# Optimization experiments

Hardware: AMD Instinct MI355X
Metric: run time of the kernel (lower is better)

## Reference

```python
import jax, jax.numpy as jnp
import numpy as np

N_NODES = 50000
N_EDGES = 1_280_000
NODE_D = 13
EDGE_RAW_D = 1
H = 64
CONCAT_D = 2 * NODE_D + EDGE_RAW_D  # 27
NEG_SLOPE = 0.2


def _leaky(x):
    return jnp.where(x >= 0, x, NEG_SLOPE * x)


def _scatter_mean(vals, idx, num_nodes):
    # vals: [E, H]; idx: [E] int -> [num_nodes, H] mean over incident edges (0 if none)
    s = jax.ops.segment_sum(vals, idx, num_segments=num_nodes)
    cnt = jax.ops.segment_sum(jnp.ones((vals.shape[0], 1), vals.dtype), idx, num_segments=num_nodes)
    return s / jnp.maximum(cnt, 1.0)


def _conv(e, src, dst, num_nodes, w_self, b_self, w_in, w_out):
    h_self = e @ w_self + b_self
    agg_in = _scatter_mean(e, dst, num_nodes)[src]   # incoming-edge mean at src nodes
    agg_out = _scatter_mean(e, src, num_nodes)[dst]  # outgoing-edge mean at dst nodes
    return _leaky(h_self + agg_in @ w_in + agg_out @ w_out)


def setup_inputs() -> dict:
    key = jax.random.key(0)
    ks = jax.random.split(key, 24)

    def lin(k, fan_in, fan_out):
        return jax.random.normal(k, (fan_in, fan_out), jnp.float32) / np.sqrt(fan_in)

    inp = {
        'x': jax.random.normal(ks[0], (N_NODES, NODE_D), jnp.float32),
        'edge_index': jax.random.randint(ks[1], (2, N_EDGES), 0, N_NODES, jnp.int32),
        'raw_edge_attr': jax.random.normal(ks[2], (N_EDGES, EDGE_RAW_D), jnp.float32),
        'enc_w': lin(ks[3], CONCAT_D, H),
        'enc_b': jnp.zeros((H,), jnp.float32),
    }
    for i, base in zip((1, 2, 3), (4, 8, 12)):
        inp[f'w_self{i}'] = lin(ks[base], H, H)
        inp[f'b_self{i}'] = jnp.zeros((H,), jnp.float32)
        inp[f'w_in{i}'] = lin(ks[base + 1], H, H)
        inp[f'w_out{i}'] = lin(ks[base + 2], H, H)
    dims = [(H, 64), (64, 64), (64, 32), (32, 1)]
    for j, (fi, fo) in enumerate(dims, start=1):
        inp[f'mlp_w{j}'] = lin(ks[15 + j], fi, fo)
        inp[f'mlp_b{j}'] = jnp.zeros((fo,), jnp.float32)
    return inp


def reference(x, edge_index, raw_edge_attr, enc_w, enc_b,
              w_self1, b_self1, w_in1, w_out1,
              w_self2, b_self2, w_in2, w_out2,
              w_self3, b_self3, w_in3, w_out3,
              mlp_w1, mlp_b1, mlp_w2, mlp_b2, mlp_w3, mlp_b3, mlp_w4, mlp_b4):
    num_nodes = x.shape[0]
    src, dst = edge_index[0], edge_index[1]
    edge_attr = jnp.concatenate([x[src], x[dst], raw_edge_attr], axis=-1)  # [E, 27]
    h = _leaky(edge_attr @ enc_w + enc_b)
    h = _conv(h, src, dst, num_nodes, w_self1, b_self1, w_in1, w_out1)
    h = _conv(h, src, dst, num_nodes, w_self2, b_self2, w_in2, w_out2)
    h = _conv(h, src, dst, num_nodes, w_self3, b_self3, w_in3, w_out3)
    h = _leaky(h @ mlp_w1 + mlp_b1)
    h = _leaky(h @ mlp_w2 + mlp_b2)
    h = _leaky(h @ mlp_w3 + mlp_b3)
    return (h @ mlp_w4 + mlp_b4).squeeze(-1)  # [E]
```

## Files before the change

kernel.cpp:

```cpp
#include <hip/hip_runtime.h>


#define NN 50000
#define NNP 50048
#define NE 1280000
#define LDP 72
#define OFFSZ 50016
#define NB 196
#define NTILES 782
#define NPX 6250

#define WAVES 2
#define EDGE_ITERS 4
#define EDGE_BLOCKS 2500

typedef unsigned int   u32;
typedef unsigned short u16;
typedef __attribute__((ext_vector_type(8))) short  short8;
typedef __attribute__((ext_vector_type(4))) float  floatx4;

#define MFMA16(a, b, c) __builtin_amdgcn_mfma_f32_16x16x32_bf16(a, b, c, 0, 0, 0)

__device__ __forceinline__ float lrelu(float x) { return x >= 0.0f ? x : 0.2f * x; }
__device__ __forceinline__ float bf2f(u16 u) { return __uint_as_float(((u32)u) << 16); }
__device__ __forceinline__ u16 f2bf(float f) {
    u32 b = __float_as_uint(f);
    return (u16)((b + 0x7FFFu + ((b >> 16) & 1u)) >> 16);
}
__device__ __forceinline__ u32 f2bf2(float lo, float hi) {
    return (u32)f2bf(lo) | ((u32)f2bf(hi) << 16);
}

__device__ __forceinline__ short8 bfrag(const float* __restrict__ W, int ld, int n, int k0) {
    short8 b;
#pragma unroll
    for (int j = 0; j < 8; ++j) b[j] = (short)f2bf(W[(k0 + j) * ld + n]);
    return b;
}

__device__ __forceinline__ void mm_tile(const u16* __restrict__ tb,
                                        const short8 wf[2][4],
                                        floatx4 acc[4][4], int c16, int q4) {
#pragma unroll
    for (int mt = 0; mt < 4; ++mt) {
        const short8 a0 = *(const short8*)(tb + (mt * 16 + c16) * LDP + q4 * 8);
        const short8 a1 = *(const short8*)(tb + (mt * 16 + c16) * LDP + 32 + q4 * 8);
#pragma unroll
        for (int nt = 0; nt < 4; ++nt) {
            acc[mt][nt] = MFMA16(a0, wf[0][nt], acc[mt][nt]);
            acc[mt][nt] = MFMA16(a1, wf[1][nt], acc[mt][nt]);
        }
    }
}

__global__ void __launch_bounds__(256)
k_bsum(const int* __restrict__ deg_in, const int* __restrict__ deg_out,
       int* __restrict__ bsum)
{
    __shared__ int s[256];
    const int tid = threadIdx.x;
    const int i = blockIdx.x * 256 + tid;
#pragma unroll 1
    for (int pass = 0; pass < 2; ++pass) {
        const int* deg = pass ? deg_out : deg_in;
        s[tid] = (i < NN) ? deg[i] : 0;
        __syncthreads();
        for (int d = 128; d > 0; d >>= 1) {
            if (tid < d) s[tid] += s[tid + d];
            __syncthreads();
        }
        if (tid == 0) bsum[pass * NB + blockIdx.x] = s[0];
        __syncthreads();
    }
}

__global__ void __launch_bounds__(256)
k_bscan(const int* __restrict__ bsum, int* __restrict__ boff)
{
    __shared__ int s[256];
    const int tid = threadIdx.x;
#pragma unroll 1
    for (int pass = 0; pass < 2; ++pass) {
        const int v = (tid < NB) ? bsum[pass * NB + tid] : 0;
        s[tid] = v;
        __syncthreads();
        for (int d = 1; d < 256; d <<= 1) {
            const int t = (tid >= d) ? s[tid - d] : 0;
            __syncthreads();
            s[tid] += t;
            __syncthreads();
        }
        if (tid < NB) boff[pass * NB + tid] = s[tid] - v;
        __syncthreads();
    }
}

__global__ void __launch_bounds__(256)
k_bfill(const int* __restrict__ deg_in, const int* __restrict__ deg_out,
        const int* __restrict__ boff,
        int* __restrict__ off_in, int* __restrict__ off_out,
        int* __restrict__ cur_in, int* __restrict__ cur_out)
{
    __shared__ int s[256];
    const int tid = threadIdx.x;
    const int i = blockIdx.x * 256 + tid;
#pragma unroll 1
    for (int pass = 0; pass < 2; ++pass) {
        const int* deg = pass ? deg_out : deg_in;
        int* off = pass ? off_out : off_in;
        int* cur = pass ? cur_out : cur_in;
        const int v = (i < NN) ? deg[i] : 0;
        s[tid] = v;
        __syncthreads();
        for (int d = 1; d < 256; d <<= 1) {
            const int t = (tid >= d) ? s[tid - d] : 0;
            __syncthreads();
            s[tid] += t;
            __syncthreads();
        }
        const int o = boff[pass * NB + blockIdx.x] + s[tid] - v;
        if (i < NN) { off[i] = o; cur[i] = o; }
        if (i == NN - 1) off[NN] = NE;
        __syncthreads();
    }
}

__global__ void __launch_bounds__(256)
k_fill(const int* __restrict__ ei, int* __restrict__ cur_in, int* __restrict__ cur_out,
       int* __restrict__ csr_in, int* __restrict__ csr_out)
{
    const int cls   = blockIdx.x & 7;
    const int slice = blockIdx.x >> 3;
    const int base  = (slice * 256 + threadIdx.x) * 8;
    const int lo = cls * NPX, hi = lo + NPX;
    int s[8], d[8];
#pragma unroll
    for (int k = 0; k < 8; ++k) s[k] = ei[base + k];
#pragma unroll
    for (int k = 0; k < 8; ++k) d[k] = ei[NE + base + k];
#pragma unroll
    for (int k = 0; k < 8; ++k)
        if (s[k] >= lo && s[k] < hi) {
            const int p = atomicAdd(&cur_out[s[k]], 1);
            csr_out[p] = base + k;
        }
#pragma unroll
    for (int k = 0; k < 8; ++k)
        if (d[k] >= lo && d[k] < hi) {
            const int q = atomicAdd(&cur_in[d[k]], 1);
            csr_in[q] = base + k;
        }
}

__global__ void __launch_bounds__(128)
k_enc(const float* __restrict__ x, const int* __restrict__ ei,
      const float* __restrict__ raw, const float* __restrict__ wenc,
      const float* __restrict__ benc, u16* __restrict__ hm,
      int* __restrict__ deg_in, int* __restrict__ deg_out)
{
    __shared__ alignas(16) u16 tile[WAVES][64 * LDP];
    const int w = threadIdx.x >> 6, lane = threadIdx.x & 63;
    const int c16 = lane & 15, q4 = lane >> 4;

    short8 wf[4];
    float bias[4];
#pragma unroll
    for (int nt = 0; nt < 4; ++nt) {
        short8 b;
#pragma unroll
        for (int j = 0; j < 8; ++j) {
            const int k = q4 * 8 + j;
            b[j] = (short)(k < 27 ? f2bf(wenc[k * 64 + nt * 16 + c16]) : 0);
        }
        wf[nt] = b;
        bias[nt] = benc[nt * 16 + c16];
    }

    for (int it = 0; it < EDGE_ITERS; ++it) {
        const int tileId = (it * EDGE_BLOCKS + blockIdx.x) * WAVES + w;
        const int e0 = tileId * 64;

        const int ms = ei[e0 + lane];
        const int md = ei[NE + e0 + lane];
        atomicAdd(&deg_out[ms], 1);
        atomicAdd(&deg_in[md], 1);

        u16* row = tile[w] + lane * LDP;
#pragma unroll
        for (int j = 0; j < 13; ++j) row[j]      = f2bf(x[ms * 13 + j]);
#pragma unroll
        for (int j = 0; j < 13; ++j) row[13 + j] = f2bf(x[md * 13 + j]);
        row[26] = f2bf(raw[e0 + lane]);
#pragma unroll
        for (int j = 27; j < 32; ++j) row[j] = 0;

#pragma unroll
        for (int mt = 0; mt < 4; ++mt) {
            const short8 a = *(const short8*)(tile[w] + (mt * 16 + c16) * LDP + q4 * 8);
            floatx4 acc[4];
#pragma unroll
            for (int nt = 0; nt < 4; ++nt) acc[nt] = (floatx4)(0.0f);
#pragma unroll
            for (int nt = 0; nt < 4; ++nt) acc[nt] = MFMA16(a, wf[nt], acc[nt]);
#pragma unroll
            for (int nt = 0; nt < 4; ++nt)
#pragma unroll
                for (int r = 0; r < 4; ++r) {
                    const int rowi = mt * 16 + q4 * 4 + r;
                    hm[(size_t)(e0 + rowi) * 64 + nt * 16 + c16] =
                        f2bf(lrelu(acc[nt][r] + bias[nt]));
                }
        }
    }
}

__global__ void __launch_bounds__(256)
k_mean(const u16* __restrict__ hm,
       const int* __restrict__ off_in, const int* __restrict__ csr_in,
       const int* __restrict__ off_out, const int* __restrict__ csr_out,
       u16* __restrict__ m_in, u16* __restrict__ m_out)
{
    const int w = threadIdx.x >> 6, lane = threadIdx.x & 63;
    const int node = blockIdx.x * 4 + w;
    const int rg = lane >> 3;
    const int co = (lane & 7) * 8;

    for (int pass = 0; pass < 2; ++pass) {
        const int* off = pass ? off_out : off_in;
        const int* csr = pass ? csr_out : csr_in;
        u16* mp        = pass ? m_out : m_in;

        const int b0 = off[node], b1 = off[node + 1];
        float fa[8], fb[8];
#pragma unroll
        for (int c = 0; c < 8; ++c) { fa[c] = 0.f; fb[c] = 0.f; }

        int j = b0;
        for (; j + 16 <= b1; j += 16) {
            const int ea = csr[j + rg];
            const int eb = csr[j + 8 + rg];
            const short8 va = *(const short8*)(hm + (size_t)ea * 64 + co);
            const short8 vb = *(const short8*)(hm + (size_t)eb * 64 + co);
#pragma unroll
            for (int c = 0; c < 8; ++c) fa[c] += bf2f((u16)va[c]);
#pragma unroll
            for (int c = 0; c < 8; ++c) fb[c] += bf2f((u16)vb[c]);
        }
        for (; j < b1; j += 8) {
            const int jj = j + rg;
            const int idx = jj < b1 ? jj : b0;
            const float fl = jj < b1 ? 1.f : 0.f;
            const int e = csr[idx];
            const short8 v = *(const short8*)(hm + (size_t)e * 64 + co);
#pragma unroll
            for (int c = 0; c < 8; ++c) fa[c] += fl * bf2f((u16)v[c]);
        }
#pragma unroll
        for (int c = 0; c < 8; ++c) fa[c] += fb[c];
#pragma unroll
        for (int d = 8; d < 64; d <<= 1)
#pragma unroll
            for (int c = 0; c < 8; ++c) fa[c] += __shfl_xor(fa[c], d, 64);

        const int deg = b1 - b0;
        const float inv = 1.0f / (float)(deg > 0 ? deg : 1);
        if (lane < 8) {
            uint4 p;
            p.x = f2bf2(fa[0] * inv, fa[1] * inv);
            p.y = f2bf2(fa[2] * inv, fa[3] * inv);
            p.z = f2bf2(fa[4] * inv, fa[5] * inv);
            p.w = f2bf2(fa[6] * inv, fa[7] * inv);
            *(uint4*)(mp + (size_t)node * 64 + lane * 8) = p;
        }
    }
}

__global__ void __launch_bounds__(256)
k_nodemm(const u16* __restrict__ m_in, const u16* __restrict__ m_out,
         const float* __restrict__ w_in, const float* __restrict__ w_out,
         u16* __restrict__ t_in, u16* __restrict__ t_out)
{
    const int w = threadIdx.x >> 6, lane = threadIdx.x & 63;
    const int c16 = lane & 15, q4 = lane >> 4;
    const int tileId = blockIdx.x * 4 + w;
    if (tileId >= NTILES) return;
    const int n0 = tileId * 64;

    for (int pass = 0; pass < 2; ++pass) {
        const u16* mp   = pass ? m_out : m_in;
        const float* wp = pass ? w_out : w_in;
        u16* tp         = pass ? t_out : t_in;

        short8 wf[2][4];
#pragma unroll
        for (int ks = 0; ks < 2; ++ks)
#pragma unroll
            for (int nt = 0; nt < 4; ++nt)
                wf[ks][nt] = bfrag(wp, 64, nt * 16 + c16, ks * 32 + q4 * 8);

#pragma unroll
        for (int mt = 0; mt < 4; ++mt) {
            const short8* ap = (const short8*)(mp + (size_t)(n0 + mt * 16 + c16) * 64 + q4 * 8);
            const short8 a0 = ap[0];
            const short8 a1 = ap[4];
            floatx4 acc[4];
#pragma unroll
            for (int nt = 0; nt < 4; ++nt) acc[nt] = (floatx4)(0.0f);
#pragma unroll
            for (int nt = 0; nt < 4; ++nt) {
                acc[nt] = MFMA16(a0, wf[0][nt], acc[nt]);
                acc[nt] = MFMA16(a1, wf[1][nt], acc[nt]);
            }
#pragma unroll
            for (int nt = 0; nt < 4; ++nt)
#pragma unroll
                for (int r = 0; r < 4; ++r) {
                    const int node = n0 + mt * 16 + q4 * 4 + r;
                    if (node < NN)
                        tp[(size_t)node * 64 + nt * 16 + c16] = f2bf(acc[nt][r]);
                }
        }
    }
}

__global__ void __launch_bounds__(128, 4)
k_edge(const float* __restrict__ wself, const float* __restrict__ bself,
       const u16* __restrict__ t_in, const u16* __restrict__ t_out,
       const int* __restrict__ ei, u16* __restrict__ hm)
{
    __shared__ int sidx[WAVES][64], didx[WAVES][64];
    const int w = threadIdx.x >> 6, lane = threadIdx.x & 63;
    const int c16 = lane & 15, q4 = lane >> 4;

    short8 wf[2][4];
    float bias[4];
#pragma unroll
    for (int ks = 0; ks < 2; ++ks)
#pragma unroll
        for (int nt = 0; nt < 4; ++nt)
            wf[ks][nt] = bfrag(wself, 64, nt * 16 + c16, ks * 32 + q4 * 8);
#pragma unroll
    for (int nt = 0; nt < 4; ++nt) bias[nt] = bself[nt * 16 + c16];

    for (int it = 0; it < EDGE_ITERS; ++it) {
        const int tileId = (it * EDGE_BLOCKS + blockIdx.x) * WAVES + w;
        const int e0 = tileId * 64;
        sidx[w][lane] = ei[e0 + lane];
        didx[w][lane] = ei[NE + e0 + lane];

#pragma unroll
        for (int mt = 0; mt < 4; ++mt) {
            const short8* ap = (const short8*)(hm + (size_t)(e0 + mt * 16 + c16) * 64 + q4 * 8);
            const short8 a0 = ap[0];
            const short8 a1 = ap[4];
            floatx4 acc[4];
#pragma unroll
            for (int nt = 0; nt < 4; ++nt) acc[nt] = (floatx4)(0.0f);
#pragma unroll
            for (int nt = 0; nt < 4; ++nt) {
                acc[nt] = MFMA16(a0, wf[0][nt], acc[nt]);
                acc[nt] = MFMA16(a1, wf[1][nt], acc[nt]);
            }
            float tv[4][4], uv[4][4];
#pragma unroll
            for (int r = 0; r < 4; ++r) {
                const int s = sidx[w][mt * 16 + q4 * 4 + r];
#pragma unroll
                for (int nt = 0; nt < 4; ++nt)
                    tv[r][nt] = bf2f(t_in[(size_t)s * 64 + nt * 16 + c16]);
            }
#pragma unroll
            for (int r = 0; r < 4; ++r) {
                const int d = didx[w][mt * 16 + q4 * 4 + r];
#pragma unroll
                for (int nt = 0; nt < 4; ++nt)
                    uv[r][nt] = bf2f(t_out[(size_t)d * 64 + nt * 16 + c16]);
            }
#pragma unroll
            for (int nt = 0; nt < 4; ++nt)
#pragma unroll
                for (int r = 0; r < 4; ++r) {
                    const int row = mt * 16 + q4 * 4 + r;
                    const float v = acc[nt][r] + bias[nt] + tv[r][nt] + uv[r][nt];
                    hm[(size_t)(e0 + row) * 64 + nt * 16 + c16] = f2bf(lrelu(v));
                }
        }
    }
}

__global__ void __launch_bounds__(128, 2)
k_edge_mlp(const float* __restrict__ wself, const float* __restrict__ bself,
           const u16* __restrict__ t_in, const u16* __restrict__ t_out,
           const int* __restrict__ ei, const u16* __restrict__ hm,
           const float* __restrict__ w1, const float* __restrict__ b1,
           const float* __restrict__ w2, const float* __restrict__ b2,
           const float* __restrict__ w3, const float* __restrict__ b3,
           const float* __restrict__ w4, const float* __restrict__ b4,
           float* __restrict__ out)
{
    __shared__ alignas(16) u16 tile[WAVES][64 * LDP];
    __shared__ int sidx[WAVES][64], didx[WAVES][64];
    const int w = threadIdx.x >> 6, lane = threadIdx.x & 63;
    const int c16 = lane & 15, q4 = lane >> 4;

    short8 wfS[2][4], wf1[2][4], wf2[2][4], wf3[2][2];
    float bS[4], bv1[4], bv2[4], bv3[2];
#pragma unroll
    for (int ks = 0; ks < 2; ++ks) {
#pragma unroll
        for (int nt = 0; nt < 4; ++nt) {
            wfS[ks][nt] = bfrag(wself, 64, nt * 16 + c16, ks * 32 + q4 * 8);
            wf1[ks][nt] = bfrag(w1,    64, nt * 16 + c16, ks * 32 + q4 * 8);
            wf2[ks][nt] = bfrag(w2,    64, nt * 16 + c16, ks * 32 + q4 * 8);
        }
#pragma unroll
        for (int nt = 0; nt < 2; ++nt)
            wf3[ks][nt] = bfrag(w3, 32, nt * 16 + c16, ks * 32 + q4 * 8);
    }
#pragma unroll
    for (int nt = 0; nt < 4; ++nt) { bS[nt] = bself[nt*16+c16]; bv1[nt] = b1[nt*16+c16]; bv2[nt] = b2[nt*16+c16]; }
#pragma unroll
    for (int nt = 0; nt < 2; ++nt) bv3[nt] = b3[nt * 16 + c16];
    const float w4a = w4[c16], w4b = w4[16 + c16], b4v = b4[0];

    for (int it = 0; it < EDGE_ITERS; ++it) {
        const int tileId = (it * EDGE_BLOCKS + blockIdx.x) * WAVES + w;
        const int e0 = tileId * 64;
        sidx[w][lane] = ei[e0 + lane];
        didx[w][lane] = ei[NE + e0 + lane];

#pragma unroll
        for (int mt = 0; mt < 4; ++mt) {
            const short8* ap = (const short8*)(hm + (size_t)(e0 + mt * 16 + c16) * 64 + q4 * 8);
            const short8 a0 = ap[0];
            const short8 a1 = ap[4];
            floatx4 acc[4];
#pragma unroll
            for (int nt = 0; nt < 4; ++nt) acc[nt] = (floatx4)(0.0f);
#pragma unroll
            for (int nt = 0; nt < 4; ++nt) {
                acc[nt] = MFMA16(a0, wfS[0][nt], acc[nt]);
                acc[nt] = MFMA16(a1, wfS[1][nt], acc[nt]);
            }
            float tv[4][4], uv[4][4];
#pragma unroll
            for (int r = 0; r < 4; ++r) {
                const int s = sidx[w][mt * 16 + q4 * 4 + r];
#pragma unroll
                for (int nt = 0; nt < 4; ++nt)
                    tv[r][nt] = bf2f(t_in[(size_t)s * 64 + nt * 16 + c16]);
            }
#pragma unroll
            for (int r = 0; r < 4; ++r) {
                const int d = didx[w][mt * 16 + q4 * 4 + r];
#pragma unroll
                for (int nt = 0; nt < 4; ++nt)
                    uv[r][nt] = bf2f(t_out[(size_t)d * 64 + nt * 16 + c16]);
            }
#pragma unroll
            for (int nt = 0; nt < 4; ++nt)
#pragma unroll
                for (int r = 0; r < 4; ++r) {
                    const int row = mt * 16 + q4 * 4 + r;
                    const float v = acc[nt][r] + bS[nt] + tv[r][nt] + uv[r][nt];
                    tile[w][row * LDP + nt * 16 + c16] = f2bf(lrelu(v));
                }
        }

        floatx4 acc[4][4];
#pragma unroll
        for (int mt = 0; mt < 4; ++mt)
#pragma unroll
            for (int nt = 0; nt < 4; ++nt) acc[mt][nt] = (floatx4)(0.0f);
        mm_tile(tile[w], wf1, acc, c16, q4);
#pragma unroll
        for (int mt = 0; mt < 4; ++mt)
#pragma unroll
            for (int nt = 0; nt < 4; ++nt)
#pragma unroll
                for (int r = 0; r < 4; ++r)
                    tile[w][(mt * 16 + q4 * 4 + r) * LDP + nt * 16 + c16] =
                        f2bf(lrelu(acc[mt][nt][r] + bv1[nt]));

#pragma unroll
        for (int mt = 0; mt < 4; ++mt)
#pragma unroll
            for (int nt = 0; nt < 4; ++nt) acc[mt][nt] = (floatx4)(0.0f);
        mm_tile(tile[w], wf2, acc, c16, q4);
#pragma unroll
        for (int mt = 0; mt < 4; ++mt)
#pragma unroll
            for (int nt = 0; nt < 4; ++nt)
#pragma unroll
                for (int r = 0; r < 4; ++r)
                    tile[w][(mt * 16 + q4 * 4 + r) * LDP + nt * 16 + c16] =
                        f2bf(lrelu(acc[mt][nt][r] + bv2[nt]));

        floatx4 a3[4][2];
#pragma unroll
        for (int mt = 0; mt < 4; ++mt)
#pragma unroll
            for (int nt = 0; nt < 2; ++nt) a3[mt][nt] = (floatx4)(0.0f);
#pragma unroll
        for (int mt = 0; mt < 4; ++mt) {
            const short8 a0 = *(const short8*)(tile[w] + (mt * 16 + c16) * LDP + q4 * 8);
            const short8 a1 = *(const short8*)(tile[w] + (mt * 16 + c16) * LDP + 32 + q4 * 8);
#pragma unroll
            for (int nt = 0; nt < 2; ++nt) {
                a3[mt][nt] = MFMA16(a0, wf3[0][nt], a3[mt][nt]);
                a3[mt][nt] = MFMA16(a1, wf3[1][nt], a3[mt][nt]);
            }
        }
#pragma unroll
        for (int mt = 0; mt < 4; ++mt)
#pragma unroll
            for (int r = 0; r < 4; ++r) {
                float p = lrelu(a3[mt][0][r] + bv3[0]) * w4a
                        + lrelu(a3[mt][1][r] + bv3[1]) * w4b;
                p += __shfl_xor(p, 1, 64);
                p += __shfl_xor(p, 2, 64);
                p += __shfl_xor(p, 4, 64);
                p += __shfl_xor(p, 8, 64);
                if (c16 == 0) out[e0 + mt * 16 + q4 * 4 + r] = p + b4v;
            }
    }
}

extern "C" void kernel_launch(void* const* d_in, const int* in_sizes, int n_in,
                              void* d_out, int out_size, void* d_ws, size_t ws_size,
                              hipStream_t stream)
{
    const float* x      = (const float*)d_in[0];
    const int*   ei     = (const int*)  d_in[1];
    const float* raw    = (const float*)d_in[2];
    const float* wenc   = (const float*)d_in[3];
    const float* benc   = (const float*)d_in[4];
    const float* wself1 = (const float*)d_in[5];
    const float* bself1 = (const float*)d_in[6];
    const float* win1   = (const float*)d_in[7];
    const float* wout1  = (const float*)d_in[8];
    const float* wself2 = (const float*)d_in[9];
    const float* bself2 = (const float*)d_in[10];
    const float* win2   = (const float*)d_in[11];
    const float* wout2  = (const float*)d_in[12];
    const float* wself3 = (const float*)d_in[13];
    const float* bself3 = (const float*)d_in[14];
    const float* win3   = (const float*)d_in[15];
    const float* wout3  = (const float*)d_in[16];
    const float* w1 = (const float*)d_in[17]; const float* b1 = (const float*)d_in[18];
    const float* w2 = (const float*)d_in[19]; const float* b2 = (const float*)d_in[20];
    const float* w3 = (const float*)d_in[21]; const float* b3 = (const float*)d_in[22];
    const float* w4 = (const float*)d_in[23]; const float* b4 = (const float*)d_in[24];

    u16*   t_in    = (u16*)d_ws;
    u16*   t_out   = t_in + (size_t)NN * 64;
    int*   deg_in  = (int*)(t_out + (size_t)NN * 64);
    int*   deg_out = deg_in + NN;
    int*   cur_in  = deg_out + NN;
    int*   cur_out = cur_in + NN;
    int*   off_in  = cur_out + NN;
    int*   off_out = off_in + OFFSZ;
    int*   csr_in  = off_out + OFFSZ;
    int*   csr_out = csr_in + NE;
    int*   bsum    = csr_out + NE;
    int*   boff    = bsum + 512;
    u16*   m_in    = (u16*)(boff + 512);
    u16*   m_out   = m_in + (size_t)NNP * 64;
    u16*   hm      = m_out + (size_t)NNP * 64;

    hipMemsetAsync(deg_in, 0, (size_t)2 * NN * sizeof(int), stream);

    k_enc<<<EDGE_BLOCKS, 128, 0, stream>>>(x, ei, raw, wenc, benc, hm, deg_in, deg_out);

    k_bsum <<<NB, 256, 0, stream>>>(deg_in, deg_out, bsum);
    k_bscan<<<1,  256, 0, stream>>>(bsum, boff);
    k_bfill<<<NB, 256, 0, stream>>>(deg_in, deg_out, boff, off_in, off_out, cur_in, cur_out);
    k_fill<<<8 * (NE / 2048), 256, 0, stream>>>(ei, cur_in, cur_out, csr_in, csr_out);

    for (int layer = 0; layer < 3; ++layer) {
        const float* wi = layer == 0 ? win1  : layer == 1 ? win2  : win3;
        const float* wo = layer == 0 ? wout1 : layer == 1 ? wout2 : wout3;
        k_mean<<<NN / 4, 256, 0, stream>>>(hm, off_in, csr_in, off_out, csr_out,
                                           m_in, m_out);
        k_nodemm<<<NB, 256, 0, stream>>>(m_in, m_out, wi, wo, t_in, t_out);
        if (layer == 0)
            k_edge<<<EDGE_BLOCKS, 128, 0, stream>>>(wself1, bself1, t_in, t_out, ei, hm);
        else if (layer == 1)
            k_edge<<<EDGE_BLOCKS, 128, 0, stream>>>(wself2, bself2, t_in, t_out, ei, hm);
        else
            k_edge_mlp<<<EDGE_BLOCKS, 128, 0, stream>>>(wself3, bself3, t_in, t_out, ei, hm,
                                                        w1, b1, w2, b2, w3, b3, w4, b4,
                                                        (float*)d_out);
    }
}
```

Before: 899.2 us.

## Permute hidden-feature layout for packed bf16 stores and pre-pack node features

Stores hidden features in a permuted column order so that each lane's four MFMA output columns are contiguous. This lets the epilogues, and the gathers from t_in/t_out, use 8-byte packed loads and stores instead of scalar 2-byte accesses. Weight fragments are loaded with the matching permutation, so the maths is unchanged. A new prep kernel converts x to bf16 rows padded to 16 elements, letting the encoder gather node features with 16-byte vector loads; this adds one small extra launch and reuses the t_in buffer as scratch.

```diff
diff --git a/kernel.cpp b/kernel.cpp
--- a/kernel.cpp
+++ b/kernel.cpp
@@ -31,10 +31,14 @@
     return (u32)f2bf(lo) | ((u32)f2bf(hi) << 16);
 }
 
-__device__ __forceinline__ short8 bfrag(const float* __restrict__ W, int ld, int n, int k0) {
+__device__ __forceinline__ short8 bfragP(const float* __restrict__ W, int ld, int n, int k0) {
     short8 b;
 #pragma unroll
-    for (int j = 0; j < 8; ++j) b[j] = (short)f2bf(W[(k0 + j) * ld + n]);
+    for (int j = 0; j < 8; ++j) {
+        const int p = k0 + j;
+        const int k = (p & 3) * 16 + (p >> 2);
+        b[j] = (short)f2bf(W[k * ld + n]);
+    }
     return b;
 }
 
@@ -51,6 +55,25 @@
             acc[mt][nt] = MFMA16(a1, wf[1][nt], acc[mt][nt]);
         }
     }
+}
+
+__global__ void __launch_bounds__(256)
+k_prep(const float* __restrict__ x, u16* __restrict__ xb)
+{
+    const int n = blockIdx.x * 256 + threadIdx.x;
+    if (n >= NN) return;
+    u16 r[16];
+#pragma unroll
+    for (int j = 0; j < 13; ++j) r[j] = f2bf(x[n * 13 + j]);
+    r[13] = 0; r[14] = 0; r[15] = 0;
+    u32 wds[8];
+#pragma unroll
+    for (int j = 0; j < 8; ++j) wds[j] = (u32)r[2 * j] | ((u32)r[2 * j + 1] << 16);
+    uint4 p0, p1;
+    p0.x = wds[0]; p0.y = wds[1]; p0.z = wds[2]; p0.w = wds[3];
+    p1.x = wds[4]; p1.y = wds[5]; p1.z = wds[6]; p1.w = wds[7];
+    *(uint4*)(xb + (size_t)n * 16)     = p0;
+    *(uint4*)(xb + (size_t)n * 16 + 8) = p1;
 }
 
 __global__ void __launch_bounds__(256)
@@ -153,7 +176,7 @@
 }
 
 __global__ void __launch_bounds__(128)
-k_enc(const float* __restrict__ x, const int* __restrict__ ei,
+k_enc(const u16* __restrict__ xb, const int* __restrict__ ei,
       const float* __restrict__ raw, const float* __restrict__ wenc,
       const float* __restrict__ benc, u16* __restrict__ hm,
       int* __restrict__ deg_in, int* __restrict__ deg_out)
@@ -169,8 +192,13 @@
         short8 b;
 #pragma unroll
         for (int j = 0; j < 8; ++j) {
-            const int k = q4 * 8 + j;
-            b[j] = (short)(k < 27 ? f2bf(wenc[k * 64 + nt * 16 + c16]) : 0);
+            const int p = q4 * 8 + j;
+            int row;
+            if (p < 13)                 row = p;
+            else if (p == 13)           row = 26;
+            else if (p >= 16 && p < 29) row = 13 + (p - 16);
+            else                        row = -1;
+            b[j] = (short)(row >= 0 ? f2bf(wenc[row * 64 + nt * 16 + c16]) : 0);
         }
         wf[nt] = b;
         bias[nt] = benc[nt * 16 + c16];
@@ -184,15 +212,18 @@
         const int md = ei[NE + e0 + lane];
         atomicAdd(&deg_out[ms], 1);
         atomicAdd(&deg_in[md], 1);
+        const float rv = raw[e0 + lane];
 
         u16* row = tile[w] + lane * LDP;
-#pragma unroll
-        for (int j = 0; j < 13; ++j) row[j]      = f2bf(x[ms * 13 + j]);
-#pragma unroll
-        for (int j = 0; j < 13; ++j) row[13 + j] = f2bf(x[md * 13 + j]);
-        row[26] = f2bf(raw[e0 + lane]);
-#pragma unroll
-        for (int j = 27; j < 32; ++j) row[j] = 0;
+        const short8 s0 = *(const short8*)(xb + (size_t)ms * 16);
+        const short8 s1 = *(const short8*)(xb + (size_t)ms * 16 + 8);
+        const short8 d0 = *(const short8*)(xb + (size_t)md * 16);
+        const short8 d1 = *(const short8*)(xb + (size_t)md * 16 + 8);
+        *(short8*)(row)      = s0;
+        *(short8*)(row + 8)  = s1;
+        *(short8*)(row + 16) = d0;
+        *(short8*)(row + 24) = d1;
+        row[13] = f2bf(rv);
 
 #pragma unroll
         for (int mt = 0; mt < 4; ++mt) {
@@ -203,13 +234,13 @@
 #pragma unroll
             for (int nt = 0; nt < 4; ++nt) acc[nt] = MFMA16(a, wf[nt], acc[nt]);
 #pragma unroll
-            for (int nt = 0; nt < 4; ++nt)
-#pragma unroll
-                for (int r = 0; r < 4; ++r) {
-                    const int rowi = mt * 16 + q4 * 4 + r;
-                    hm[(size_t)(e0 + rowi) * 64 + nt * 16 + c16] =
-                        f2bf(lrelu(acc[nt][r] + bias[nt]));
-                }
+            for (int r = 0; r < 4; ++r) {
+                const int rowi = mt * 16 + q4 * 4 + r;
+                uint2 pkt;
+                pkt.x = f2bf2(lrelu(acc[0][r] + bias[0]), lrelu(acc[1][r] + bias[1]));
+                pkt.y = f2bf2(lrelu(acc[2][r] + bias[2]), lrelu(acc[3][r] + bias[3]));
+                *(uint2*)(hm + (size_t)(e0 + rowi) * 64 + c16 * 4) = pkt;
+            }
         }
     }
 }
@@ -296,7 +327,7 @@
         for (int ks = 0; ks < 2; ++ks)
 #pragma unroll
             for (int nt = 0; nt < 4; ++nt)
-                wf[ks][nt] = bfrag(wp, 64, nt * 16 + c16, ks * 32 + q4 * 8);
+                wf[ks][nt] = bfragP(wp, 64, nt * 16 + c16, ks * 32 + q4 * 8);
 
 #pragma unroll
         for (int mt = 0; mt < 4; ++mt) {
@@ -312,13 +343,15 @@
                 acc[nt] = MFMA16(a1, wf[1][nt], acc[nt]);
             }
 #pragma unroll
-            for (int nt = 0; nt < 4; ++nt)
-#pragma unroll
-                for (int r = 0; r < 4; ++r) {
-                    const int node = n0 + mt * 16 + q4 * 4 + r;
-                    if (node < NN)
-                        tp[(size_t)node * 64 + nt * 16 + c16] = f2bf(acc[nt][r]);
+            for (int r = 0; r < 4; ++r) {
+                const int node = n0 + mt * 16 + q4 * 4 + r;
+                if (node < NN) {
+                    uint2 pkt;
+                    pkt.x = f2bf2(acc[0][r], acc[1][r]);
+                    pkt.y = f2bf2(acc[2][r], acc[3][r]);
+                    *(uint2*)(tp + (size_t)node * 64 + c16 * 4) = pkt;
                 }
+            }
         }
     }
 }
@@ -338,7 +371,7 @@
     for (int ks = 0; ks < 2; ++ks)
 #pragma unroll
         for (int nt = 0; nt < 4; ++nt)
-            wf[ks][nt] = bfrag(wself, 64, nt * 16 + c16, ks * 32 + q4 * 8);
+            wf[ks][nt] = bfragP(wself, 64, nt * 16 + c16, ks * 32 + q4 * 8);
 #pragma unroll
     for (int nt = 0; nt < 4; ++nt) bias[nt] = bself[nt * 16 + c16];
 
@@ -365,25 +398,27 @@
 #pragma unroll
             for (int r = 0; r < 4; ++r) {
                 const int s = sidx[w][mt * 16 + q4 * 4 + r];
-#pragma unroll
-                for (int nt = 0; nt < 4; ++nt)
-                    tv[r][nt] = bf2f(t_in[(size_t)s * 64 + nt * 16 + c16]);
+                const uint2 v = *(const uint2*)(t_in + (size_t)s * 64 + c16 * 4);
+                tv[r][0] = bf2f((u16)v.x); tv[r][1] = bf2f((u16)(v.x >> 16));
+                tv[r][2] = bf2f((u16)v.y); tv[r][3] = bf2f((u16)(v.y >> 16));
             }
 #pragma unroll
             for (int r = 0; r < 4; ++r) {
                 const int d = didx[w][mt * 16 + q4 * 4 + r];
-#pragma unroll
-                for (int nt = 0; nt < 4; ++nt)
-                    uv[r][nt] = bf2f(t_out[(size_t)d * 64 + nt * 16 + c16]);
-            }
-#pragma unroll
-            for (int nt = 0; nt < 4; ++nt)
-#pragma unroll
-                for (int r = 0; r < 4; ++r) {
-                    const int row = mt * 16 + q4 * 4 + r;
-                    const float v = acc[nt][r] + bias[nt] + tv[r][nt] + uv[r][nt];
-                    hm[(size_t)(e0 + row) * 64 + nt * 16 + c16] = f2bf(lrelu(v));
-                }
+                const uint2 v = *(const uint2*)(t_out + (size_t)d * 64 + c16 * 4);
+                uv[r][0] = bf2f((u16)v.x); uv[r][1] = bf2f((u16)(v.x >> 16));
+                uv[r][2] = bf2f((u16)v.y); uv[r][3] = bf2f((u16)(v.y >> 16));
+            }
+#pragma unroll
+            for (int r = 0; r < 4; ++r) {
+                const int row = mt * 16 + q4 * 4 + r;
+                const float v0 = lrelu(acc[0][r] + bias[0] + tv[r][0] + uv[r][0]);
+                const float v1 = lrelu(acc[1][r] + bias[1] + tv[r][1] + uv[r][1]);
+                const float v2 = lrelu(acc[2][r] + bias[2] + tv[r][2] + uv[r][2]);
+                const float v3 = lrelu(acc[3][r] + bias[3] + tv[r][3] + uv[r][3]);
+                uint2 pkt; pkt.x = f2bf2(v0, v1); pkt.y = f2bf2(v2, v3);
+                *(uint2*)(hm + (size_t)(e0 + row) * 64 + c16 * 4) = pkt;
+            }
         }
     }
 }
@@ -409,13 +444,13 @@
     for (int ks = 0; ks < 2; ++ks) {
 #pragma unroll
         for (int nt = 0; nt < 4; ++nt) {
-            wfS[ks][nt] = bfrag(wself, 64, nt * 16 + c16, ks * 32 + q4 * 8);
-            wf1[ks][nt] = bfrag(w1,    64, nt * 16 + c16, ks * 32 + q4 * 8);
-            wf2[ks][nt] = bfrag(w2,    64, nt * 16 + c16, ks * 32 + q4 * 8);
+            wfS[ks][nt] = bfragP(wself, 64, nt * 16 + c16, ks * 32 + q4 * 8);
+            wf1[ks][nt] = bfragP(w1,    64, nt * 16 + c16, ks * 32 + q4 * 8);
+            wf2[ks][nt] = bfragP(w2,    64, nt * 16 + c16, ks * 32 + q4 * 8);
         }
 #pragma unroll
         for (int nt = 0; nt < 2; ++nt)
-            wf3[ks][nt] = bfrag(w3, 32, nt * 16 + c16, ks * 32 + q4 * 8);
+            wf3[ks][nt] = bfragP(w3, 32, nt * 16 + c16, ks * 32 + q4 * 8);
     }
 #pragma unroll
     for (int nt = 0; nt < 4; ++nt) { bS[nt] = bself[nt*16+c16]; bv1[nt] = b1[nt*16+c16]; bv2[nt] = b2[nt*16+c16]; }
@@ -446,25 +481,27 @@
 #pragma unroll
             for (int r = 0; r < 4; ++r) {
                 const int s = sidx[w][mt * 16 + q4 * 4 + r];
-#pragma unroll
-                for (int nt = 0; nt < 4; ++nt)
-                    tv[r][nt] = bf2f(t_in[(size_t)s * 64 + nt * 16 + c16]);
+                const uint2 v = *(const uint2*)(t_in + (size_t)s * 64 + c16 * 4);
+                tv[r][0] = bf2f((u16)v.x); tv[r][1] = bf2f((u16)(v.x >> 16));
+                tv[r][2] = bf2f((u16)v.y); tv[r][3] = bf2f((u16)(v.y >> 16));
             }
 #pragma unroll
             for (int r = 0; r < 4; ++r) {
                 const int d = didx[w][mt * 16 + q4 * 4 + r];
-#pragma unroll
-                for (int nt = 0; nt < 4; ++nt)
-                    uv[r][nt] = bf2f(t_out[(size_t)d * 64 + nt * 16 + c16]);
-            }
-#pragma unroll
-            for (int nt = 0; nt < 4; ++nt)
-#pragma unroll
-                for (int r = 0; r < 4; ++r) {
-                    const int row = mt * 16 + q4 * 4 + r;
-                    const float v = acc[nt][r] + bS[nt] + tv[r][nt] + uv[r][nt];
-                    tile[w][row * LDP + nt * 16 + c16] = f2bf(lrelu(v));
-                }
+                const uint2 v = *(const uint2*)(t_out + (size_t)d * 64 + c16 * 4);
+                uv[r][0] = bf2f((u16)v.x); uv[r][1] = bf2f((u16)(v.x >> 16));
+                uv[r][2] = bf2f((u16)v.y); uv[r][3] = bf2f((u16)(v.y >> 16));
+            }
+#pragma unroll
+            for (int r = 0; r < 4; ++r) {
+                const int row = mt * 16 + q4 * 4 + r;
+                const float v0 = lrelu(acc[0][r] + bS[0] + tv[r][0] + uv[r][0]);
+                const float v1 = lrelu(acc[1][r] + bS[1] + tv[r][1] + uv[r][1]);
+                const float v2 = lrelu(acc[2][r] + bS[2] + tv[r][2] + uv[r][2]);
+                const float v3 = lrelu(acc[3][r] + bS[3] + tv[r][3] + uv[r][3]);
+                uint2 pkt; pkt.x = f2bf2(v0, v1); pkt.y = f2bf2(v2, v3);
+                *(uint2*)(tile[w] + row * LDP + c16 * 4) = pkt;
+            }
         }
 
         floatx4 acc[4][4];
@@ -476,11 +513,13 @@
 #pragma unroll
         for (int mt = 0; mt < 4; ++mt)
 #pragma unroll
-            for (int nt = 0; nt < 4; ++nt)
-#pragma unroll
-                for (int r = 0; r < 4; ++r)
-                    tile[w][(mt * 16 + q4 * 4 + r) * LDP + nt * 16 + c16] =
-                        f2bf(lrelu(acc[mt][nt][r] + bv1[nt]));
+            for (int r = 0; r < 4; ++r) {
+                const int row = mt * 16 + q4 * 4 + r;
+                uint2 pkt;
+                pkt.x = f2bf2(lrelu(acc[mt][0][r] + bv1[0]), lrelu(acc[mt][1][r] + bv1[1]));
+                pkt.y = f2bf2(lrelu(acc[mt][2][r] + bv1[2]), lrelu(acc[mt][3][r] + bv1[3]));
+                *(uint2*)(tile[w] + row * LDP + c16 * 4) = pkt;
+            }
 
 #pragma unroll
         for (int mt = 0; mt < 4; ++mt)
@@ -490,11 +529,13 @@
 #pragma unroll
         for (int mt = 0; mt < 4; ++mt)
 #pragma unroll
-            for (int nt = 0; nt < 4; ++nt)
-#pragma unroll
-                for (int r = 0; r < 4; ++r)
-                    tile[w][(mt * 16 + q4 * 4 + r) * LDP + nt * 16 + c16] =
-                        f2bf(lrelu(acc[mt][nt][r] + bv2[nt]));
+            for (int r = 0; r < 4; ++r) {
+                const int row = mt * 16 + q4 * 4 + r;
+                uint2 pkt;
+                pkt.x = f2bf2(lrelu(acc[mt][0][r] + bv2[0]), lrelu(acc[mt][1][r] + bv2[1]));
+                pkt.y = f2bf2(lrelu(acc[mt][2][r] + bv2[2]), lrelu(acc[mt][3][r] + bv2[3]));
+                *(uint2*)(tile[w] + row * LDP + c16 * 4) = pkt;
+            }
 
         floatx4 a3[4][2];
 #pragma unroll
@@ -568,9 +609,13 @@
     u16*   m_out   = m_in + (size_t)NNP * 64;
     u16*   hm      = m_out + (size_t)NNP * 64;
 
+    u16*   xb      = t_in;
+
     hipMemsetAsync(deg_in, 0, (size_t)2 * NN * sizeof(int), stream);
 
-    k_enc<<<EDGE_BLOCKS, 128, 0, stream>>>(x, ei, raw, wenc, benc, hm, deg_in, deg_out);
+    k_prep<<<NB, 256, 0, stream>>>(x, xb);
+
+    k_enc<<<EDGE_BLOCKS, 128, 0, stream>>>(xb, ei, raw, wenc, benc, hm, deg_in, deg_out);
 
     k_bsum <<<NB, 256, 0, stream>>>(deg_in, deg_out, bsum);
     k_bscan<<<1,  256, 0, stream>>>(bsum, boff);
```

After: 866.8 us. 3.6% less time.
